# Performance work log

Measured on AMD Instinct MI355X. Metric: run time of the kernel, lower is better.

## Reference

```python
import jax, jax.numpy as jnp
import numpy as np

N = 50000
E = 800000
D_IN = 128
HID = 128
L = 3


def setup_inputs() -> dict:
    key = jax.random.key(0)
    ks = jax.random.split(key, 16)
    s = 0.05
    return {
        "x": jax.random.normal(ks[0], (N, D_IN), jnp.float32),
        "edge_attr": jax.random.normal(ks[1], (E, 1), jnp.float32),
        "edge_index": jax.random.randint(ks[2], (2, E), 0, N, jnp.int64),
        # stacked per-layer GINEConv params (all layers have in=out=128)
        "Wl1": jax.random.normal(ks[3], (L, D_IN, HID), jnp.float32) * s,
        "bl1": jax.random.normal(ks[4], (L, HID), jnp.float32) * s,
        "Wl2": jax.random.normal(ks[5], (L, HID, HID), jnp.float32) * s,
        "bl2": jax.random.normal(ks[6], (L, HID), jnp.float32) * s,
        # edge_attr linear: edge_dim=1 -> in_channels of each layer's nn
        "We": jax.random.normal(ks[7], (L, 1, D_IN), jnp.float32) * s,
        "be": jax.random.normal(ks[8], (L, D_IN), jnp.float32) * s,
        # edge predictor MLP: Linear(2*HID, HID) -> ReLU -> (Dropout: eval) -> Linear(HID, 1)
        "Wp1": jax.random.normal(ks[9], (2 * HID, HID), jnp.float32) * s,
        "bp1": jax.random.normal(ks[10], (HID,), jnp.float32) * s,
        "Wp2": jax.random.normal(ks[11], (HID, 1), jnp.float32) * s,
        "bp2": jax.random.normal(ks[12], (1,), jnp.float32) * s,
    }


def reference(x, edge_attr, edge_index, Wl1, bl1, Wl2, bl2, We, be, Wp1, bp1, Wp2, bp2):
    src, dst = edge_index[0], edge_index[1]  # PyG: row=source j, col=target i
    n = x.shape[0]
    for l in range(Wl1.shape[0]):
        # GINEConv message: ReLU(x_j + Lin(edge_attr)); sum-aggregate into target i
        msg = jax.nn.relu(x[src] + edge_attr @ We[l] + be[l])        # [E, D]
        aggr = jax.ops.segment_sum(msg, dst, num_segments=n)         # [N, D]
        # out = nn((1+eps)*x + aggr), eps=0; nn = Lin->ReLU->Lin; then outer ReLU
        h = jax.nn.relu((x + aggr) @ Wl1[l] + bl1[l])
        x = jax.nn.relu(h @ Wl2[l] + bl2[l])
    edge_feat = jnp.concatenate([x[src], x[dst]], axis=1)            # [E, 2*HID]
    h = jax.nn.relu(edge_feat @ Wp1 + bp1)                           # dropout = identity (eval)
    return (h @ Wp2 + bp2).squeeze(-1)                               # [E]
```

## Files before the change

### kernel.cpp

```cpp
#include <hip/hip_runtime.h>

#define NN 50000
#define NE 800000
#define DD 128

typedef __attribute__((ext_vector_type(8))) short short8;
typedef __attribute__((ext_vector_type(4))) float f32x4;

__device__ inline unsigned short f2bf_rne(float f) {
  unsigned u = __float_as_uint(f);
  u += 0x7FFF + ((u >> 16) & 1);
  return (unsigned short)(u >> 16);
}
__device__ inline float bf2f(unsigned short h) {
  return __uint_as_float(((unsigned)h) << 16);
}

__global__ __launch_bounds__(256) void hist_rank(const int* __restrict__ dst,
                                                 int* __restrict__ cnt,
                                                 int* __restrict__ rank) {
  int e = blockIdx.x * 256 + threadIdx.x;
  if (e < NE) rank[e] = atomicAdd(&cnt[dst[e]], 1);
}

__global__ __launch_bounds__(1024) void scan_nodes(const int* __restrict__ cnt,
                                                   int* __restrict__ offs) {
  __shared__ int wsum[16];
  __shared__ int wpre[16];
  const int t = threadIdx.x;
  const int lane = t & 63, wv = t >> 6;
  int carry = 0;
  for (int base = 0; base < NN; base += 8192) {
    const int i0 = base + t * 8;
    int4 a = make_int4(0, 0, 0, 0), b = make_int4(0, 0, 0, 0);
    if (i0 + 8 <= NN) {
      a = *(const int4*)(cnt + i0);
      b = *(const int4*)(cnt + i0 + 4);
    } else if (i0 < NN) {
      int tmp[8];
      for (int j = 0; j < 8; ++j) tmp[j] = (i0 + j < NN) ? cnt[i0 + j] : 0;
      a = make_int4(tmp[0], tmp[1], tmp[2], tmp[3]);
      b = make_int4(tmp[4], tmp[5], tmp[6], tmp[7]);
    }
    const int own = a.x + a.y + a.z + a.w + b.x + b.y + b.z + b.w;
    int inc = own;
#pragma unroll
    for (int d = 1; d < 64; d <<= 1) {
      int v = __shfl_up(inc, d, 64);
      if (lane >= d) inc += v;
    }
    if (lane == 63) wsum[wv] = inc;
    __syncthreads();
    if (t < 16) {
      int v = wsum[t];
      int p = v;
#pragma unroll
      for (int d = 1; d < 16; d <<= 1) {
        int u = __shfl_up(p, d, 16);
        if (t >= d) p += u;
      }
      wpre[t] = p - v;
      if (t == 15) wsum[15] = p;
    }
    __syncthreads();
    int run = carry + wpre[wv] + inc - own;
    const int o0 = run,      o1 = o0 + a.x, o2 = o1 + a.y, o3 = o2 + a.z;
    const int o4 = o3 + a.w, o5 = o4 + b.x, o6 = o5 + b.y, o7 = o6 + b.z;
    if (i0 + 8 <= NN) {
      *(int4*)(offs + i0)     = make_int4(o0, o1, o2, o3);
      *(int4*)(offs + i0 + 4) = make_int4(o4, o5, o6, o7);
    } else if (i0 < NN) {
      const int o[8] = {o0, o1, o2, o3, o4, o5, o6, o7};
      for (int j = 0; j < 8; ++j)
        if (i0 + j < NN) offs[i0 + j] = o[j];
    }
    carry += wsum[15];
    __syncthreads();
  }
  if (t == 0) offs[NN] = carry;
}

__global__ __launch_bounds__(256) void csr_fill(
    const int* __restrict__ src, const int* __restrict__ dst,
    const float* __restrict__ ea, const int* __restrict__ offs,
    const int* __restrict__ rank, int4* __restrict__ recs) {
  int e = blockIdx.x * 256 + threadIdx.x;
  if (e >= NE) return;
  int pos = offs[dst[e]] + rank[e];
  recs[pos] = make_int4(src[e], e, __float_as_int(ea[e]), 0);
}

__global__ __launch_bounds__(256) void prep_w(
    const float* __restrict__ Wl1, const float* __restrict__ Wl2,
    const float* __restrict__ Wp1,
    unsigned short* __restrict__ WTh, unsigned short* __restrict__ WTl) {
  int tid = blockIdx.x * 256 + threadIdx.x;
  if (tid >= 8 * 16384) return;
  int g = tid >> 14, idx = tid & 16383;
  int n = idx >> 7, k = idx & 127;
  const float* s;
  if (g < 3) s = Wl1 + (size_t)g * 16384;
  else if (g < 6) s = Wl2 + (size_t)(g - 3) * 16384;
  else s = Wp1 + (size_t)(g - 6) * 16384;
  float v = s[k * 128 + n];
  unsigned short hi = f2bf_rne(v);
  WTh[tid] = hi;
  WTl[tid] = f2bf_rne(v - bf2f(hi));
}

__global__ __launch_bounds__(256) void cvt_bf(const float2* __restrict__ in,
                                              unsigned* __restrict__ out, int n2) {
  int i = blockIdx.x * 256 + threadIdx.x;
  if (i < n2) {
    float2 v = in[i];
    out[i] = (unsigned)f2bf_rne(v.x) | ((unsigned)f2bf_rne(v.y) << 16);
  }
}

__global__ __launch_bounds__(256) void aggregate(
    const float* __restrict__ x, const unsigned short* __restrict__ xbf,
    const int* __restrict__ offs, const int4* __restrict__ recs,
    const float4* __restrict__ We4, const float4* __restrict__ be4,
    float* __restrict__ out) {
  const int slot = threadIdx.x >> 5, lane = threadIdx.x & 31;
  const int n = blockIdx.x * 8 + slot;
  if (n >= NN) return;
  const float4 wv = We4[lane], bv = be4[lane];
  float4 a0 = ((const float4*)(x + (size_t)n * DD))[lane];
  float4 a1 = make_float4(0.f, 0.f, 0.f, 0.f);
  float4 a2 = make_float4(0.f, 0.f, 0.f, 0.f);
  float4 a3 = make_float4(0.f, 0.f, 0.f, 0.f);
  const int beg = offs[n], end = offs[n + 1];
  int i = beg;
#define GATH(acc, rec)                                                        \
  {                                                                           \
    const float ee = __int_as_float((rec).z);                                 \
    const uint2 qq = *(const uint2*)(xbf + (size_t)(rec).x * DD + lane * 4);  \
    const float g0 = __uint_as_float(qq.x << 16);                             \
    const float g1 = __uint_as_float(qq.x & 0xffff0000u);                     \
    const float g2 = __uint_as_float(qq.y << 16);                             \
    const float g3 = __uint_as_float(qq.y & 0xffff0000u);                     \
    acc.x += fmaxf(fmaf(ee, wv.x, bv.x) + g0, 0.f);                           \
    acc.y += fmaxf(fmaf(ee, wv.y, bv.y) + g1, 0.f);                           \
    acc.z += fmaxf(fmaf(ee, wv.z, bv.z) + g2, 0.f);                           \
    acc.w += fmaxf(fmaf(ee, wv.w, bv.w) + g3, 0.f);                           \
  }
  for (; i + 4 <= end; i += 4) {
    const int4 r0 = recs[i], r1 = recs[i + 1], r2 = recs[i + 2], r3 = recs[i + 3];
    GATH(a0, r0)
    GATH(a1, r1)
    GATH(a2, r2)
    GATH(a3, r3)
  }
  for (; i < end; ++i) {
    const int4 r0 = recs[i];
    GATH(a0, r0)
  }
#undef GATH
  a0.x += a1.x + a2.x + a3.x;
  a0.y += a1.y + a2.y + a3.y;
  a0.z += a1.z + a2.z + a3.z;
  a0.w += a1.w + a2.w + a3.w;
  ((float4*)(out + (size_t)n * DD))[lane] = a0;
}

template <bool DUALBF>
__global__ __launch_bounds__(256) void fused_mlp(
    const float* __restrict__ in,
    const unsigned short* __restrict__ W1h, const unsigned short* __restrict__ W1l,
    const unsigned short* __restrict__ W2h, const unsigned short* __restrict__ W2l,
    const float* __restrict__ b1, const float* __restrict__ b2,
    float* __restrict__ out, unsigned short* __restrict__ outbf) {
  __shared__ float hl[16][132];
  const int t = threadIdx.x;
  const int w = t >> 6, l = t & 63;
  const int lr = l & 15, kg = l >> 4;

  short8 B1h_[2][4], B1l_[2][4], B2h_[2][4], B2l_[2][4];
#pragma unroll
  for (int ct = 0; ct < 2; ++ct)
#pragma unroll
    for (int ks = 0; ks < 4; ++ks) {
      const size_t bo = (size_t)((w * 2 + ct) * 16 + lr) * DD + ks * 32 + kg * 8;
      B1h_[ct][ks] = *(const short8*)(W1h + bo);
      B1l_[ct][ks] = *(const short8*)(W1l + bo);
      B2h_[ct][ks] = *(const short8*)(W2h + bo);
      B2l_[ct][ks] = *(const short8*)(W2l + bo);
    }
  const float b1v0 = b1[(w * 2 + 0) * 16 + lr];
  const float b1v1 = b1[(w * 2 + 1) * 16 + lr];
  const float b2v0 = b2[(w * 2 + 0) * 16 + lr];
  const float b2v1 = b2[(w * 2 + 1) * 16 + lr];

  for (int c = blockIdx.x; c < NN / 16; c += gridDim.x) {
    f32x4 acc[2];
    {
      const float* ap = in + ((size_t)c * 16 + lr) * DD + kg * 8;
      float va[4][8];
#pragma unroll
      for (int ks = 0; ks < 4; ++ks) {
        *(float4*)&va[ks][0] = *(const float4*)(ap + ks * 32);
        *(float4*)&va[ks][4] = *(const float4*)(ap + ks * 32 + 4);
      }
      short8 ah[4], al[4];
#pragma unroll
      for (int ks = 0; ks < 4; ++ks)
#pragma unroll
        for (int j = 0; j < 8; ++j) {
          unsigned short h = f2bf_rne(va[ks][j]);
          ah[ks][j] = (short)h;
          al[ks][j] = (short)f2bf_rne(va[ks][j] - bf2f(h));
        }
      acc[0] = (f32x4){0.f, 0.f, 0.f, 0.f};
      acc[1] = (f32x4){0.f, 0.f, 0.f, 0.f};
#pragma unroll
      for (int ks = 0; ks < 4; ++ks)
#pragma unroll
        for (int ct = 0; ct < 2; ++ct) {
          acc[ct] = __builtin_amdgcn_mfma_f32_16x16x32_bf16(ah[ks], B1h_[ct][ks], acc[ct], 0, 0, 0);
          acc[ct] = __builtin_amdgcn_mfma_f32_16x16x32_bf16(ah[ks], B1l_[ct][ks], acc[ct], 0, 0, 0);
          acc[ct] = __builtin_amdgcn_mfma_f32_16x16x32_bf16(al[ks], B1h_[ct][ks], acc[ct], 0, 0, 0);
        }
    }
    __syncthreads();
#pragma unroll
    for (int ct = 0; ct < 2; ++ct) {
      const float bb = ct ? b1v1 : b1v0;
      const int col = (w * 2 + ct) * 16 + lr;
#pragma unroll
      for (int q = 0; q < 4; ++q)
        hl[kg * 4 + q][col] = fmaxf(acc[ct][q] + bb, 0.f);
    }
    __syncthreads();
    {
      float va[4][8];
#pragma unroll
      for (int ks = 0; ks < 4; ++ks) {
        *(float4*)&va[ks][0] = *(const float4*)&hl[lr][ks * 32 + kg * 8];
        *(float4*)&va[ks][4] = *(const float4*)&hl[lr][ks * 32 + kg * 8 + 4];
      }
      short8 ah[4], al[4];
#pragma unroll
      for (int ks = 0; ks < 4; ++ks)
#pragma unroll
        for (int j = 0; j < 8; ++j) {
          unsigned short h = f2bf_rne(va[ks][j]);
          ah[ks][j] = (short)h;
          al[ks][j] = (short)f2bf_rne(va[ks][j] - bf2f(h));
        }
      acc[0] = (f32x4){0.f, 0.f, 0.f, 0.f};
      acc[1] = (f32x4){0.f, 0.f, 0.f, 0.f};
#pragma unroll
      for (int ks = 0; ks < 4; ++ks)
#pragma unroll
        for (int ct = 0; ct < 2; ++ct) {
          acc[ct] = __builtin_amdgcn_mfma_f32_16x16x32_bf16(ah[ks], B2h_[ct][ks], acc[ct], 0, 0, 0);
          acc[ct] = __builtin_amdgcn_mfma_f32_16x16x32_bf16(ah[ks], B2l_[ct][ks], acc[ct], 0, 0, 0);
          acc[ct] = __builtin_amdgcn_mfma_f32_16x16x32_bf16(al[ks], B2h_[ct][ks], acc[ct], 0, 0, 0);
        }
    }
#pragma unroll
    for (int ct = 0; ct < 2; ++ct) {
      const float bb = ct ? b2v1 : b2v0;
      const int col = (w * 2 + ct) * 16 + lr;
#pragma unroll
      for (int q = 0; q < 4; ++q) {
        const float v = fmaxf(acc[ct][q] + bb, 0.f);
        const size_t r = (size_t)c * 16 + kg * 4 + q;
        out[r * DD + col] = v;
        if (DUALBF) outbf[r * DD + col] = f2bf_rne(v);
      }
    }
  }
}

__global__ __launch_bounds__(256) void gemm_pred2(
    const float* __restrict__ in,
    const unsigned short* __restrict__ W1h, const unsigned short* __restrict__ W1l,
    const unsigned short* __restrict__ W2h, const unsigned short* __restrict__ W2l,
    const float* __restrict__ bp1,
    unsigned short* __restrict__ P1bf, float* __restrict__ P2) {
  const int t = threadIdx.x;
  const int w = t >> 6, l = t & 63;
  const int lr = l & 15, kg = l >> 4;

  short8 B1h[2][4], B1l[2][4], B2h[2][4], B2l[2][4];
#pragma unroll
  for (int ct = 0; ct < 2; ++ct)
#pragma unroll
    for (int ks = 0; ks < 4; ++ks) {
      const size_t bo = (size_t)((w * 2 + ct) * 16 + lr) * DD + ks * 32 + kg * 8;
      B1h[ct][ks] = *(const short8*)(W1h + bo);
      B1l[ct][ks] = *(const short8*)(W1l + bo);
      B2h[ct][ks] = *(const short8*)(W2h + bo);
      B2l[ct][ks] = *(const short8*)(W2l + bo);
    }
  float bv0 = bp1[(w * 2 + 0) * 16 + lr];
  float bv1 = bp1[(w * 2 + 1) * 16 + lr];

  for (int c = blockIdx.x; c < NN / 16; c += gridDim.x) {
    const float* ap = in + ((size_t)c * 16 + lr) * DD + kg * 8;
    float va[4][8];
#pragma unroll
    for (int ks = 0; ks < 4; ++ks) {
      *(float4*)&va[ks][0] = *(const float4*)(ap + ks * 32);
      *(float4*)&va[ks][4] = *(const float4*)(ap + ks * 32 + 4);
    }
    short8 ah[4], al[4];
#pragma unroll
    for (int ks = 0; ks < 4; ++ks)
#pragma unroll
      for (int j = 0; j < 8; ++j) {
        unsigned short h = f2bf_rne(va[ks][j]);
        ah[ks][j] = (short)h;
        al[ks][j] = (short)f2bf_rne(va[ks][j] - bf2f(h));
      }
    f32x4 acc1[2], acc2[2];
    acc1[0] = (f32x4){0.f, 0.f, 0.f, 0.f};
    acc1[1] = (f32x4){0.f, 0.f, 0.f, 0.f};
    acc2[0] = (f32x4){0.f, 0.f, 0.f, 0.f};
    acc2[1] = (f32x4){0.f, 0.f, 0.f, 0.f};
#pragma unroll
    for (int ks = 0; ks < 4; ++ks) {
#pragma unroll
      for (int ct = 0; ct < 2; ++ct) {
        acc1[ct] = __builtin_amdgcn_mfma_f32_16x16x32_bf16(ah[ks], B1h[ct][ks], acc1[ct], 0, 0, 0);
        acc1[ct] = __builtin_amdgcn_mfma_f32_16x16x32_bf16(ah[ks], B1l[ct][ks], acc1[ct], 0, 0, 0);
        acc1[ct] = __builtin_amdgcn_mfma_f32_16x16x32_bf16(al[ks], B1h[ct][ks], acc1[ct], 0, 0, 0);
        acc2[ct] = __builtin_amdgcn_mfma_f32_16x16x32_bf16(ah[ks], B2h[ct][ks], acc2[ct], 0, 0, 0);
        acc2[ct] = __builtin_amdgcn_mfma_f32_16x16x32_bf16(ah[ks], B2l[ct][ks], acc2[ct], 0, 0, 0);
        acc2[ct] = __builtin_amdgcn_mfma_f32_16x16x32_bf16(al[ks], B2h[ct][ks], acc2[ct], 0, 0, 0);
      }
    }
    __syncthreads();
#pragma unroll
    for (int ct = 0; ct < 2; ++ct) {
      const int col = (w * 2 + ct) * 16 + lr;
      const float bb = ct ? bv1 : bv0;
#pragma unroll
      for (int q4 = 0; q4 < 4; ++q4) {
        const size_t r = (size_t)c * 16 + kg * 4 + q4;
        P1bf[r * DD + col] = f2bf_rne(acc1[ct][q4]);
        P2[r * DD + col] = acc2[ct][q4] + bb;
      }
    }
  }
}

__global__ __launch_bounds__(256) void edge_out(
    const unsigned short* __restrict__ P1bf, const float4* __restrict__ P2_4,
    const int* __restrict__ offs, const int4* __restrict__ recs,
    const float4* __restrict__ Wp2_4,
    const float* __restrict__ bp2, float* __restrict__ out) {
  const int slot = threadIdx.x >> 5, lane = threadIdx.x & 31;
  const int n = blockIdx.x * 8 + slot;
  if (n >= NN) return;
  const float4 w = Wp2_4[lane];
  const float bb = bp2[0];
  const float4 p2 = P2_4[(size_t)n * 32 + lane];
  const int beg = offs[n], end = offs[n + 1];
  int i = beg;
  for (; i + 4 <= end; i += 4) {
    float v[4];
    int eid[4];
#pragma unroll
    for (int u = 0; u < 4; ++u) {
      const int4 rec = recs[i + u];
      eid[u] = rec.y;
      const uint2 qq = *(const uint2*)(P1bf + (size_t)rec.x * DD + lane * 4);
      const float q0 = __uint_as_float(qq.x << 16);
      const float q1 = __uint_as_float(qq.x & 0xffff0000u);
      const float q2 = __uint_as_float(qq.y << 16);
      const float q3 = __uint_as_float(qq.y & 0xffff0000u);
      v[u] = fmaxf(q0 + p2.x, 0.f) * w.x + fmaxf(q1 + p2.y, 0.f) * w.y
           + fmaxf(q2 + p2.z, 0.f) * w.z + fmaxf(q3 + p2.w, 0.f) * w.w;
    }
#pragma unroll
    for (int m = 16; m >= 1; m >>= 1) {
#pragma unroll
      for (int u = 0; u < 4; ++u) v[u] += __shfl_xor(v[u], m, 64);
    }
    if (lane == 0) {
#pragma unroll
      for (int u = 0; u < 4; ++u) out[eid[u]] = v[u] + bb;
    }
  }
  for (; i < end; ++i) {
    const int4 rec = recs[i];
    const uint2 qq = *(const uint2*)(P1bf + (size_t)rec.x * DD + lane * 4);
    const float q0 = __uint_as_float(qq.x << 16);
    const float q1 = __uint_as_float(qq.x & 0xffff0000u);
    const float q2 = __uint_as_float(qq.y << 16);
    const float q3 = __uint_as_float(qq.y & 0xffff0000u);
    float v = fmaxf(q0 + p2.x, 0.f) * w.x + fmaxf(q1 + p2.y, 0.f) * w.y
            + fmaxf(q2 + p2.z, 0.f) * w.z + fmaxf(q3 + p2.w, 0.f) * w.w;
#pragma unroll
    for (int m = 16; m >= 1; m >>= 1) v += __shfl_xor(v, m, 64);
    if (lane == 0) out[rec.y] = v + bb;
  }
}

extern "C" void kernel_launch(void* const* d_in, const int* in_sizes, int n_in,
                              void* d_out, int out_size, void* d_ws, size_t ws_size,
                              hipStream_t stream) {
  const float* x_in = (const float*)d_in[0];
  const float* ea   = (const float*)d_in[1];
  const int*   ei   = (const int*)d_in[2];
  const float* Wl1 = (const float*)d_in[3];
  const float* bl1 = (const float*)d_in[4];
  const float* Wl2 = (const float*)d_in[5];
  const float* bl2 = (const float*)d_in[6];
  const float* We  = (const float*)d_in[7];
  const float* be  = (const float*)d_in[8];
  const float* Wp1 = (const float*)d_in[9];
  const float* bp1 = (const float*)d_in[10];
  const float* Wp2 = (const float*)d_in[11];
  const float* bp2 = (const float*)d_in[12];
  const int* src = ei;
  const int* dst = ei + NE;

  float* bufA   = (float*)d_ws;
  float* bufB   = bufA + (size_t)NN * DD;
  int*   cnt    = (int*)(bufB + (size_t)NN * DD);
  int*   offs   = cnt + NN;
  int*   rank   = offs + NN + 1;
  int4*  recs   = (int4*)(((uintptr_t)(rank + NE) + 15) & ~(uintptr_t)15);
  unsigned short* WTh = (unsigned short*)(recs + NE);
  unsigned short* WTl = WTh + 8 * 16384;
  unsigned short* xbf = WTl + 8 * 16384;

  hipMemsetAsync(cnt, 0, NN * sizeof(int), stream);
  hist_rank<<<NE / 256, 256, 0, stream>>>(dst, cnt, rank);
  scan_nodes<<<1, 1024, 0, stream>>>(cnt, offs);
  csr_fill<<<NE / 256, 256, 0, stream>>>(src, dst, ea, offs, rank, recs);
  prep_w<<<(8 * 16384 + 255) / 256, 256, 0, stream>>>(Wl1, Wl2, Wp1, WTh, WTl);
  cvt_bf<<<(NN * DD / 2 + 255) / 256, 256, 0, stream>>>(
      (const float2*)x_in, (unsigned*)xbf, NN * DD / 2);

  const int GB = 1024;
  const int AB = (NN + 7) / 8;
#define WH(g) (WTh + (size_t)(g) * 16384)
#define WL(g) (WTl + (size_t)(g) * 16384)

  aggregate<<<AB, 256, 0, stream>>>(
      x_in, xbf, offs, recs, (const float4*)We, (const float4*)be, bufA);
  fused_mlp<true><<<GB, 256, 0, stream>>>(
      bufA, WH(0), WL(0), WH(3), WL(3), bl1, bl2, bufB, xbf);
  aggregate<<<AB, 256, 0, stream>>>(
      bufB, xbf, offs, recs, (const float4*)(We + DD), (const float4*)(be + DD), bufA);
  fused_mlp<true><<<GB, 256, 0, stream>>>(
      bufA, WH(1), WL(1), WH(4), WL(4), bl1 + DD, bl2 + DD, bufB, xbf);
  aggregate<<<AB, 256, 0, stream>>>(
      bufB, xbf, offs, recs, (const float4*)(We + 2 * DD), (const float4*)(be + 2 * DD), bufA);
  fused_mlp<false><<<GB, 256, 0, stream>>>(
      bufA, WH(2), WL(2), WH(5), WL(5), bl1 + 2 * DD, bl2 + 2 * DD, bufB, nullptr);
  gemm_pred2<<<GB, 256, 0, stream>>>(bufB, WH(6), WL(6), WH(7), WL(7), bp1,
                                     (unsigned short*)bufA, bufB);
  edge_out<<<AB, 256, 0, stream>>>(
      (const unsigned short*)bufA, (const float4*)bufB, offs, recs,
      (const float4*)Wp2, bp2, (float*)d_out);
}
```

Measured before the change: 408.2 us.

## Fuse prologue kernels, deepen gather unrolling, store P2 as bf16

Merges the memset, weight-transpose and x-to-bf16 conversion into one prologue kernel to cut launch overhead. The aggregate and edge_out gathers are restructured to issue 8 record loads and then 8 row loads before any arithmetic, so more memory requests are in flight per warp. P2 from gemm_pred2 is written as bf16 into the xbf buffer instead of fp32, halving that traffic at some precision cost. A __syncthreads in gemm_pred2 is also removed.

```diff
diff --git a/kernel.cpp b/kernel.cpp
--- a/kernel.cpp
+++ b/kernel.cpp
@@ -14,6 +14,32 @@
 }
 __device__ inline float bf2f(unsigned short h) {
   return __uint_as_float(((unsigned)h) << 16);
+}
+
+__global__ __launch_bounds__(256) void prologue(
+    const float* __restrict__ Wl1, const float* __restrict__ Wl2,
+    const float* __restrict__ Wp1,
+    unsigned short* __restrict__ WTh, unsigned short* __restrict__ WTl,
+    const float2* __restrict__ xin2, unsigned* __restrict__ xbf2,
+    int* __restrict__ cnt) {
+  const int tid = blockIdx.x * 256 + threadIdx.x;
+  if (tid < NN) cnt[tid] = 0;
+  if (tid < 8 * 16384) {
+    const int g = tid >> 14, idx = tid & 16383;
+    const int n = idx >> 7, k = idx & 127;
+    const float* s;
+    if (g < 3) s = Wl1 + (size_t)g * 16384;
+    else if (g < 6) s = Wl2 + (size_t)(g - 3) * 16384;
+    else s = Wp1 + (size_t)(g - 6) * 16384;
+    const float v = s[k * 128 + n];
+    const unsigned short hi = f2bf_rne(v);
+    WTh[tid] = hi;
+    WTl[tid] = f2bf_rne(v - bf2f(hi));
+  }
+  if (tid < NN * DD / 2) {
+    const float2 v = xin2[tid];
+    xbf2[tid] = (unsigned)f2bf_rne(v.x) | ((unsigned)f2bf_rne(v.y) << 16);
+  }
 }
 
 __global__ __launch_bounds__(256) void hist_rank(const int* __restrict__ dst,
@@ -90,33 +116,6 @@
   recs[pos] = make_int4(src[e], e, __float_as_int(ea[e]), 0);
 }
 
-__global__ __launch_bounds__(256) void prep_w(
-    const float* __restrict__ Wl1, const float* __restrict__ Wl2,
-    const float* __restrict__ Wp1,
-    unsigned short* __restrict__ WTh, unsigned short* __restrict__ WTl) {
-  int tid = blockIdx.x * 256 + threadIdx.x;
-  if (tid >= 8 * 16384) return;
-  int g = tid >> 14, idx = tid & 16383;
-  int n = idx >> 7, k = idx & 127;
-  const float* s;
-  if (g < 3) s = Wl1 + (size_t)g * 16384;
-  else if (g < 6) s = Wl2 + (size_t)(g - 3) * 16384;
-  else s = Wp1 + (size_t)(g - 6) * 16384;
-  float v = s[k * 128 + n];
-  unsigned short hi = f2bf_rne(v);
-  WTh[tid] = hi;
-  WTl[tid] = f2bf_rne(v - bf2f(hi));
-}
-
-__global__ __launch_bounds__(256) void cvt_bf(const float2* __restrict__ in,
-                                              unsigned* __restrict__ out, int n2) {
-  int i = blockIdx.x * 256 + threadIdx.x;
-  if (i < n2) {
-    float2 v = in[i];
-    out[i] = (unsigned)f2bf_rne(v.x) | ((unsigned)f2bf_rne(v.y) << 16);
-  }
-}
-
 __global__ __launch_bounds__(256) void aggregate(
     const float* __restrict__ x, const unsigned short* __restrict__ xbf,
     const int* __restrict__ offs, const int4* __restrict__ recs,
@@ -132,31 +131,45 @@
   float4 a3 = make_float4(0.f, 0.f, 0.f, 0.f);
   const int beg = offs[n], end = offs[n + 1];
   int i = beg;
-#define GATH(acc, rec)                                                        \
+#define ACCQ(acc, rec, qq)                                                    \
   {                                                                           \
     const float ee = __int_as_float((rec).z);                                 \
-    const uint2 qq = *(const uint2*)(xbf + (size_t)(rec).x * DD + lane * 4);  \
-    const float g0 = __uint_as_float(qq.x << 16);                             \
-    const float g1 = __uint_as_float(qq.x & 0xffff0000u);                     \
-    const float g2 = __uint_as_float(qq.y << 16);                             \
-    const float g3 = __uint_as_float(qq.y & 0xffff0000u);                     \
+    const float g0 = __uint_as_float((qq).x << 16);                           \
+    const float g1 = __uint_as_float((qq).x & 0xffff0000u);                   \
+    const float g2 = __uint_as_float((qq).y << 16);                           \
+    const float g3 = __uint_as_float((qq).y & 0xffff0000u);                   \
     acc.x += fmaxf(fmaf(ee, wv.x, bv.x) + g0, 0.f);                           \
     acc.y += fmaxf(fmaf(ee, wv.y, bv.y) + g1, 0.f);                           \
     acc.z += fmaxf(fmaf(ee, wv.z, bv.z) + g2, 0.f);                           \
     acc.w += fmaxf(fmaf(ee, wv.w, bv.w) + g3, 0.f);                           \
   }
+  for (; i + 8 <= end; i += 8) {
+    int4 r[8];
+#pragma unroll
+    for (int u = 0; u < 8; ++u) r[u] = recs[i + u];
+    uint2 q[8];
+#pragma unroll
+    for (int u = 0; u < 8; ++u)
+      q[u] = *(const uint2*)(xbf + (size_t)r[u].x * DD + lane * 4);
+    ACCQ(a0, r[0], q[0]) ACCQ(a1, r[1], q[1]) ACCQ(a2, r[2], q[2]) ACCQ(a3, r[3], q[3])
+    ACCQ(a0, r[4], q[4]) ACCQ(a1, r[5], q[5]) ACCQ(a2, r[6], q[6]) ACCQ(a3, r[7], q[7])
+  }
   for (; i + 4 <= end; i += 4) {
-    const int4 r0 = recs[i], r1 = recs[i + 1], r2 = recs[i + 2], r3 = recs[i + 3];
-    GATH(a0, r0)
-    GATH(a1, r1)
-    GATH(a2, r2)
-    GATH(a3, r3)
+    int4 r[4];
+#pragma unroll
+    for (int u = 0; u < 4; ++u) r[u] = recs[i + u];
+    uint2 q[4];
+#pragma unroll
+    for (int u = 0; u < 4; ++u)
+      q[u] = *(const uint2*)(xbf + (size_t)r[u].x * DD + lane * 4);
+    ACCQ(a0, r[0], q[0]) ACCQ(a1, r[1], q[1]) ACCQ(a2, r[2], q[2]) ACCQ(a3, r[3], q[3])
   }
   for (; i < end; ++i) {
     const int4 r0 = recs[i];
-    GATH(a0, r0)
-  }
-#undef GATH
+    const uint2 q0 = *(const uint2*)(xbf + (size_t)r0.x * DD + lane * 4);
+    ACCQ(a0, r0, q0)
+  }
+#undef ACCQ
   a0.x += a1.x + a2.x + a3.x;
   a0.y += a1.y + a2.y + a3.y;
   a0.z += a1.z + a2.z + a3.z;
@@ -279,7 +292,7 @@
     const unsigned short* __restrict__ W1h, const unsigned short* __restrict__ W1l,
     const unsigned short* __restrict__ W2h, const unsigned short* __restrict__ W2l,
     const float* __restrict__ bp1,
-    unsigned short* __restrict__ P1bf, float* __restrict__ P2) {
+    unsigned short* __restrict__ P1bf, unsigned short* __restrict__ P2bf) {
   const int t = threadIdx.x;
   const int w = t >> 6, l = t & 63;
   const int lr = l & 15, kg = l >> 4;
@@ -332,7 +345,6 @@
         acc2[ct] = __builtin_amdgcn_mfma_f32_16x16x32_bf16(al[ks], B2h[ct][ks], acc2[ct], 0, 0, 0);
       }
     }
-    __syncthreads();
 #pragma unroll
     for (int ct = 0; ct < 2; ++ct) {
       const int col = (w * 2 + ct) * 16 + lr;
@@ -341,14 +353,14 @@
       for (int q4 = 0; q4 < 4; ++q4) {
         const size_t r = (size_t)c * 16 + kg * 4 + q4;
         P1bf[r * DD + col] = f2bf_rne(acc1[ct][q4]);
-        P2[r * DD + col] = acc2[ct][q4] + bb;
+        P2bf[r * DD + col] = f2bf_rne(acc2[ct][q4] + bb);
       }
     }
   }
 }
 
 __global__ __launch_bounds__(256) void edge_out(
-    const unsigned short* __restrict__ P1bf, const float4* __restrict__ P2_4,
+    const unsigned short* __restrict__ P1bf, const unsigned short* __restrict__ P2bf,
     const int* __restrict__ offs, const int4* __restrict__ recs,
     const float4* __restrict__ Wp2_4,
     const float* __restrict__ bp2, float* __restrict__ out) {
@@ -357,24 +369,55 @@
   if (n >= NN) return;
   const float4 w = Wp2_4[lane];
   const float bb = bp2[0];
-  const float4 p2 = P2_4[(size_t)n * 32 + lane];
+  const uint2 pq = *(const uint2*)(P2bf + (size_t)n * DD + lane * 4);
+  float4 p2;
+  p2.x = __uint_as_float(pq.x << 16);
+  p2.y = __uint_as_float(pq.x & 0xffff0000u);
+  p2.z = __uint_as_float(pq.y << 16);
+  p2.w = __uint_as_float(pq.y & 0xffff0000u);
   const int beg = offs[n], end = offs[n + 1];
   int i = beg;
+#define EDGEV(vv, qq)                                                         \
+  {                                                                           \
+    const float q0 = __uint_as_float((qq).x << 16);                           \
+    const float q1 = __uint_as_float((qq).x & 0xffff0000u);                   \
+    const float q2 = __uint_as_float((qq).y << 16);                           \
+    const float q3 = __uint_as_float((qq).y & 0xffff0000u);                   \
+    vv = fmaxf(q0 + p2.x, 0.f) * w.x + fmaxf(q1 + p2.y, 0.f) * w.y            \
+       + fmaxf(q2 + p2.z, 0.f) * w.z + fmaxf(q3 + p2.w, 0.f) * w.w;           \
+  }
+  for (; i + 8 <= end; i += 8) {
+    int4 r[8];
+#pragma unroll
+    for (int u = 0; u < 8; ++u) r[u] = recs[i + u];
+    uint2 q[8];
+#pragma unroll
+    for (int u = 0; u < 8; ++u)
+      q[u] = *(const uint2*)(P1bf + (size_t)r[u].x * DD + lane * 4);
+    float v[8];
+#pragma unroll
+    for (int u = 0; u < 8; ++u) EDGEV(v[u], q[u])
+#pragma unroll
+    for (int m = 16; m >= 1; m >>= 1) {
+#pragma unroll
+      for (int u = 0; u < 8; ++u) v[u] += __shfl_xor(v[u], m, 64);
+    }
+    if (lane == 0) {
+#pragma unroll
+      for (int u = 0; u < 8; ++u) out[r[u].y] = v[u] + bb;
+    }
+  }
   for (; i + 4 <= end; i += 4) {
+    int4 r[4];
+#pragma unroll
+    for (int u = 0; u < 4; ++u) r[u] = recs[i + u];
+    uint2 q[4];
+#pragma unroll
+    for (int u = 0; u < 4; ++u)
+      q[u] = *(const uint2*)(P1bf + (size_t)r[u].x * DD + lane * 4);
     float v[4];
-    int eid[4];
-#pragma unroll
-    for (int u = 0; u < 4; ++u) {
-      const int4 rec = recs[i + u];
-      eid[u] = rec.y;
-      const uint2 qq = *(const uint2*)(P1bf + (size_t)rec.x * DD + lane * 4);
-      const float q0 = __uint_as_float(qq.x << 16);
-      const float q1 = __uint_as_float(qq.x & 0xffff0000u);
-      const float q2 = __uint_as_float(qq.y << 16);
-      const float q3 = __uint_as_float(qq.y & 0xffff0000u);
-      v[u] = fmaxf(q0 + p2.x, 0.f) * w.x + fmaxf(q1 + p2.y, 0.f) * w.y
-           + fmaxf(q2 + p2.z, 0.f) * w.z + fmaxf(q3 + p2.w, 0.f) * w.w;
-    }
+#pragma unroll
+    for (int u = 0; u < 4; ++u) EDGEV(v[u], q[u])
 #pragma unroll
     for (int m = 16; m >= 1; m >>= 1) {
 #pragma unroll
@@ -382,22 +425,19 @@
     }
     if (lane == 0) {
 #pragma unroll
-      for (int u = 0; u < 4; ++u) out[eid[u]] = v[u] + bb;
+      for (int u = 0; u < 4; ++u) out[r[u].y] = v[u] + bb;
     }
   }
   for (; i < end; ++i) {
     const int4 rec = recs[i];
     const uint2 qq = *(const uint2*)(P1bf + (size_t)rec.x * DD + lane * 4);
-    const float q0 = __uint_as_float(qq.x << 16);
-    const float q1 = __uint_as_float(qq.x & 0xffff0000u);
-    const float q2 = __uint_as_float(qq.y << 16);
-    const float q3 = __uint_as_float(qq.y & 0xffff0000u);
-    float v = fmaxf(q0 + p2.x, 0.f) * w.x + fmaxf(q1 + p2.y, 0.f) * w.y
-            + fmaxf(q2 + p2.z, 0.f) * w.z + fmaxf(q3 + p2.w, 0.f) * w.w;
+    float v;
+    EDGEV(v, qq)
 #pragma unroll
     for (int m = 16; m >= 1; m >>= 1) v += __shfl_xor(v, m, 64);
     if (lane == 0) out[rec.y] = v + bb;
   }
+#undef EDGEV
 }
 
 extern "C" void kernel_launch(void* const* d_in, const int* in_sizes, int n_in,
@@ -429,13 +469,11 @@
   unsigned short* WTl = WTh + 8 * 16384;
   unsigned short* xbf = WTl + 8 * 16384;
 
-  hipMemsetAsync(cnt, 0, NN * sizeof(int), stream);
+  prologue<<<(NN * DD / 2 + 255) / 256, 256, 0, stream>>>(
+      Wl1, Wl2, Wp1, WTh, WTl, (const float2*)x_in, (unsigned*)xbf, cnt);
   hist_rank<<<NE / 256, 256, 0, stream>>>(dst, cnt, rank);
   scan_nodes<<<1, 1024, 0, stream>>>(cnt, offs);
   csr_fill<<<NE / 256, 256, 0, stream>>>(src, dst, ea, offs, rank, recs);
-  prep_w<<<(8 * 16384 + 255) / 256, 256, 0, stream>>>(Wl1, Wl2, Wp1, WTh, WTl);
-  cvt_bf<<<(NN * DD / 2 + 255) / 256, 256, 0, stream>>>(
-      (const float2*)x_in, (unsigned*)xbf, NN * DD / 2);
 
   const int GB = 1024;
   const int AB = (NN + 7) / 8;
@@ -455,8 +493,8 @@
   fused_mlp<false><<<GB, 256, 0, stream>>>(
       bufA, WH(2), WL(2), WH(5), WL(5), bl1 + 2 * DD, bl2 + 2 * DD, bufB, nullptr);
   gemm_pred2<<<GB, 256, 0, stream>>>(bufB, WH(6), WL(6), WH(7), WL(7), bp1,
-                                     (unsigned short*)bufA, bufB);
+                                     (unsigned short*)bufA, xbf);
   edge_out<<<AB, 256, 0, stream>>>(
-      (const unsigned short*)bufA, (const float4*)bufB, offs, recs,
+      (const unsigned short*)bufA, xbf, offs, recs,
       (const float4*)Wp2, bp2, (float*)d_out);
 }
```

Result: faster. 397.1 us (-2.7%).
